# Optimization experiments

Hardware: AMD Instinct MI355X
Metric: run time of the kernel (lower is better)

The kernel has to match this reference:

```python
import jax, jax.numpy as jnp
import numpy as np

EMBED = 1024
HEADS = 16
HEAD_DIM = EMBED // HEADS
LN_EPS = 1e-5


def setup_inputs() -> dict:
    key = jax.random.key(0)
    ks = jax.random.split(key, 12)
    B, LQ, LK = 2, 2048, 2048
    s = 1.0 / np.sqrt(EMBED)
    inp = {
        "query_seq": jax.random.normal(ks[0], (B, LQ, EMBED), jnp.float32),
        "key_value_seq": jax.random.normal(ks[1], (B, LK, EMBED), jnp.float32),
        "prompt_size": 0,
        "Wq": jax.random.normal(ks[2], (EMBED, EMBED), jnp.float32) * s,
        "bq": jnp.zeros((EMBED,), jnp.float32),
        "Wk": jax.random.normal(ks[3], (EMBED, EMBED), jnp.float32) * s,
        "bk": jnp.zeros((EMBED,), jnp.float32),
        "Wv": jax.random.normal(ks[4], (EMBED, EMBED), jnp.float32) * s,
        "bv": jnp.zeros((EMBED,), jnp.float32),
        "Wo": jax.random.normal(ks[5], (EMBED, EMBED), jnp.float32) * s,
        "bo": jnp.zeros((EMBED,), jnp.float32),
        "ln_gamma": jnp.ones((EMBED,), jnp.float32),
        "ln_beta": jnp.zeros((EMBED,), jnp.float32),
    }
    return inp


def _split_heads(x):
    B, L, _ = x.shape
    return x.reshape(B, L, HEADS, HEAD_DIM).transpose(0, 2, 1, 3)  # [B,H,L,Dh]


def reference(query_seq, key_value_seq, prompt_size, Wq, bq, Wk, bk, Wv, bv, Wo, bo, ln_gamma, ln_beta):
    # projections (torch nn.Linear: x @ W.T + b)
    q = _split_heads(query_seq @ Wq.T + bq)
    k = _split_heads(key_value_seq @ Wk.T + bk)
    v = _split_heads(key_value_seq @ Wv.T + bv)
    # naive attention: full score matrix, softmax over keys
    scores = jnp.einsum("bhqd,bhkd->bhqk", q, k) / np.sqrt(HEAD_DIM).astype(np.float32)
    attn = jax.nn.softmax(scores, axis=-1)
    ctx = jnp.einsum("bhqk,bhkd->bhqd", attn, v)
    B, H, LQ, Dh = ctx.shape
    ctx = ctx.transpose(0, 2, 1, 3).reshape(B, LQ, H * Dh)
    out = ctx @ Wo.T + bo
    # residual + LayerNorm
    x = out + query_seq
    mu = jnp.mean(x, axis=-1, keepdims=True)
    var = jnp.var(x, axis=-1, keepdims=True)
    return (x - mu) * jax.lax.rsqrt(var + LN_EPS) * ln_gamma + ln_beta
```

## Files before the change

### kernel.cpp

```cpp
#include <hip/hip_runtime.h>

typedef unsigned short u16;
typedef unsigned int u32;
typedef __attribute__((ext_vector_type(8))) __bf16 bf16x8;
typedef __attribute__((ext_vector_type(4))) float f32x4;
typedef __attribute__((ext_vector_type(16))) float f32x16;

#define EMBED 1024
#define NB 2
#define LQ 2048
#define HEADS 16
#define DH 64
#define QSCALE 0.18033688011112042f

__device__ __forceinline__ u16 f2bf(float f) {
  u32 u = __float_as_uint(f);
  u32 r = (u + 0x7FFFu + ((u >> 16) & 1u)) >> 16;
  return (u16)r;
}

__device__ __forceinline__ void glds16(const void* g, void* l) {
  __builtin_amdgcn_global_load_lds((const __attribute__((address_space(1))) void*)g,
                                   (__attribute__((address_space(3))) void*)l, 16, 0, 0);
}

__device__ __forceinline__ f32x4 mfma16(bf16x8 a, bf16x8 b, f32x4 c) {
  return __builtin_amdgcn_mfma_f32_16x16x32_bf16(a, b, c, 0, 0, 0);
}
__device__ __forceinline__ f32x16 mfma32(bf16x8 a, bf16x8 b, f32x16 c) {
  return __builtin_amdgcn_mfma_f32_32x32x16_bf16(a, b, c, 0, 0, 0);
}

__device__ __forceinline__ void pl32(u32& a, u32& b) {
  asm("v_permlane32_swap_b32 %0, %1" : "+v"(a), "+v"(b));
}

__device__ __forceinline__ u32 packbf(float a, float b) {
  return __builtin_amdgcn_perm(__float_as_uint(b), __float_as_uint(a), 0x07060302u);
}

__global__ __launch_bounds__(256) void cast_kernel(
    const float* __restrict__ q, const float* __restrict__ kv,
    const float* __restrict__ wq, const float* __restrict__ wk,
    const float* __restrict__ wv, const float* __restrict__ wo,
    u16* __restrict__ qb, u16* __restrict__ kvb, u16* __restrict__ wqb,
    u16* __restrict__ wkb, u16* __restrict__ wvb, u16* __restrict__ wob) {
  int bid = blockIdx.x;
  const float* src;
  u16* dst;
  long base;
  if (bid < 2048) {
    src = q; dst = qb; base = (long)bid * 2048;
  } else if (bid < 4096) {
    src = kv; dst = kvb; base = (long)(bid - 2048) * 2048;
  } else {
    int wsel = (bid - 4096) >> 9;
    int wb = (bid - 4096) & 511;
    if (wsel == 0) { src = wq; dst = wqb; }
    else if (wsel == 1) { src = wk; dst = wkb; }
    else if (wsel == 2) { src = wv; dst = wvb; }
    else { src = wo; dst = wob; }
    base = (long)wb * 2048;
  }
  long e = base + (long)threadIdx.x * 8;
  float4 f0 = *(const float4*)(src + e);
  float4 f1 = *(const float4*)(src + e + 4);
  uint4 o;
  o.x = (u32)f2bf(f0.x) | ((u32)f2bf(f0.y) << 16);
  o.y = (u32)f2bf(f0.z) | ((u32)f2bf(f0.w) << 16);
  o.z = (u32)f2bf(f1.x) | ((u32)f2bf(f1.y) << 16);
  o.w = (u32)f2bf(f1.z) | ((u32)f2bf(f1.w) << 16);
  *(uint4*)(dst + e) = o;
}

template <int IT>
__device__ __forceinline__ void gemm_core(
    u16* As, u16* Bs, const u16* __restrict__ A, const u16* __restrict__ W,
    const float* __restrict__ bias, const float* __restrict__ resid,
    void* __restrict__ outp, int mode, int bx, int by) {
  const int K = EMBED;
  const int TM = IT * 32;
  const int tid = threadIdx.x;
  const int lane = tid & 63;
  const int wv = tid >> 6;
  const int wm = wv >> 1, wn = wv & 1;
  const int l16 = lane & 15, quad = lane >> 4;
  const long tile_m = (long)bx * TM;
  const long tile_n = (long)by * 128;

  f32x4 z4 = {0.f, 0.f, 0.f, 0.f};
  f32x4 acc[IT][4];
#pragma unroll
  for (int i = 0; i < IT; i++)
#pragma unroll
    for (int j = 0; j < 4; j++) acc[i][j] = z4;

  for (int k0 = 0; k0 < K; k0 += 64) {
#pragma unroll
    for (int it = 0; it < TM / 32; it++) {
      int lin = it * 256 + tid;
      int row = lin >> 3, cc = lin & 7;
      glds16(A + (tile_m + row) * K + k0 + ((cc ^ (row & 7)) << 3), As + lin * 8);
    }
#pragma unroll
    for (int it = 0; it < 4; it++) {
      int lin = it * 256 + tid;
      int row = lin >> 3, cc = lin & 7;
      glds16(W + (tile_n + row) * K + k0 + ((cc ^ (row & 7)) << 3), Bs + lin * 8);
    }
    __syncthreads();
    bf16x8 af[IT][2], bfr[4][2];
#pragma unroll
    for (int i = 0; i < IT; i++) {
      int row = wm * (IT * 16) + i * 16 + l16;
#pragma unroll
      for (int ki = 0; ki < 2; ki++)
        af[i][ki] = *(const bf16x8*)(As + row * 64 + (((ki * 4 + quad) ^ (row & 7)) << 3));
    }
#pragma unroll
    for (int j = 0; j < 4; j++) {
      int row = wn * 64 + j * 16 + l16;
#pragma unroll
      for (int ki = 0; ki < 2; ki++)
        bfr[j][ki] = *(const bf16x8*)(Bs + row * 64 + (((ki * 4 + quad) ^ (row & 7)) << 3));
    }
#pragma unroll
    for (int ki = 0; ki < 2; ki++)
#pragma unroll
      for (int i = 0; i < IT; i++)
#pragma unroll
        for (int j = 0; j < 4; j++) acc[i][j] = mfma16(af[i][ki], bfr[j][ki], acc[i][j]);
    __syncthreads();
  }

#pragma unroll
  for (int j = 0; j < 4; j++) {
    int gn = (int)tile_n + wn * 64 + j * 16 + l16;
    float bv = bias[gn];
#pragma unroll
    for (int i = 0; i < IT; i++) {
      long gm0 = tile_m + wm * (IT * 16) + i * 16 + quad * 4;
      if (mode == 3) {
#pragma unroll
        for (int r = 0; r < 4; r++) {
          long idx = (gm0 + r) * EMBED + gn;
          ((float*)outp)[idx] = acc[i][j][r] + bv + resid[idx];
        }
      } else if (mode == 2) {
        int b = (int)(gm0 >> 11), l = (int)(gm0 & 2047);
        int hh = gn >> 6, dh = gn & 63;
        uint2 pk;
        pk.x = (u32)f2bf(acc[i][j][0] + bv) | ((u32)f2bf(acc[i][j][1] + bv) << 16);
        pk.y = (u32)f2bf(acc[i][j][2] + bv) | ((u32)f2bf(acc[i][j][3] + bv) << 16);
        *(uint2*)((u16*)outp + (long)((b * HEADS + hh) * DH + dh) * LQ + l) = pk;
      } else {
#pragma unroll
        for (int r = 0; r < 4; r++) {
          long gm = gm0 + r;
          float v = acc[i][j][r] + bv;
          if (mode == 0) v *= QSCALE;
          int b = (int)(gm >> 11), l = (int)(gm & 2047);
          int hh = gn >> 6, dh = gn & 63;
          ((u16*)outp)[(long)((b * HEADS + hh) * LQ + l) * DH + dh] = f2bf(v);
        }
      }
    }
  }
}

__global__ __launch_bounds__(256) void qkv_kernel(
    const u16* __restrict__ qb, const u16* __restrict__ kvb,
    const u16* __restrict__ wqb, const u16* __restrict__ wkb, const u16* __restrict__ wvb,
    const float* __restrict__ bq, const float* __restrict__ bk, const float* __restrict__ bv,
    u16* __restrict__ Qh, u16* __restrict__ Kh, u16* __restrict__ Vt) {
  __shared__ u16 As[128 * 64];
  __shared__ u16 Bs[128 * 64];
  if (blockIdx.z == 0)      gemm_core<4>(As, Bs, qb,  wqb, bq, nullptr, Qh, 0, blockIdx.x, blockIdx.y);
  else if (blockIdx.z == 1) gemm_core<4>(As, Bs, kvb, wkb, bk, nullptr, Kh, 1, blockIdx.x, blockIdx.y);
  else                      gemm_core<4>(As, Bs, kvb, wvb, bv, nullptr, Vt, 2, blockIdx.x, blockIdx.y);
}

__global__ __launch_bounds__(256) void oproj_kernel(
    const u16* __restrict__ ctx, const u16* __restrict__ wob,
    const float* __restrict__ bo, const float* __restrict__ resid, float* __restrict__ out) {
  __shared__ u16 As[64 * 64];
  __shared__ u16 Bs[128 * 64];
  gemm_core<2>(As, Bs, ctx, wob, bo, resid, out, 3, blockIdx.x, blockIdx.y);
}

__global__ __launch_bounds__(256, 2) void attn_kernel(
    const u16* __restrict__ Qh, const u16* __restrict__ Kh,
    const u16* __restrict__ Vt, u16* __restrict__ ctx) {
  __shared__ u16 Qs[128 * 64];
  __shared__ u16 KVs[3][2][64 * 64];
  const int tid = threadIdx.x;
  const int lane = tid & 63;
  const int wv = tid >> 6;
  const int l32 = lane & 31, h = lane >> 5;
  const int qt = blockIdx.x, bh = blockIdx.y;
  const long qoff = (long)bh * (LQ * DH) + (long)qt * (128 * DH);
  const long koff = (long)bh * (LQ * DH);
  const long voff = (long)bh * (DH * LQ);
  const int qbase = wv * 32;

#define STAGE_KV(t, N)                                                          \
  do {                                                                          \
    _Pragma("unroll") for (int it = 0; it < 2; it++) {                          \
      int lin = it * 256 + tid;                                                 \
      int row = lin >> 3, cc = lin & 7;                                         \
      glds16(Kh + koff + (long)((t) * 64 + row) * 64 + ((cc ^ (row & 7)) << 3), \
             &KVs[N][0][0] + lin * 8);                                          \
      glds16(Vt + voff + (long)row * LQ + (t) * 64 + ((cc ^ (row & 7)) << 3),   \
             &KVs[N][1][0] + lin * 8);                                          \
    }                                                                           \
  } while (0)

#pragma unroll
  for (int it = 0; it < 4; it++) {
    int lin = it * 256 + tid;
    int row = lin >> 3, cc = lin & 7;
    glds16(Qh + qoff + row * 64 + ((cc ^ (row & 7)) << 3), Qs + lin * 8);
  }
  STAGE_KV(0, 0);
  STAGE_KV(1, 1);
  __syncthreads();

  bf16x8 bq[4];
  {
    int row = qbase + l32;
#pragma unroll
    for (int ks = 0; ks < 4; ks++)
      bq[ks] = *(const bf16x8*)(Qs + row * 64 + (((ks * 2 + h) ^ (row & 7)) << 3));
  }

  f32x16 z16 = {0.f, 0.f, 0.f, 0.f, 0.f, 0.f, 0.f, 0.f,
                0.f, 0.f, 0.f, 0.f, 0.f, 0.f, 0.f, 0.f};
  f32x16 ot[2];
  ot[0] = z16;
  ot[1] = z16;
  f32x16 st[2];
  uint2 pk[2][4];
  float2 ls2 = {0.f, 0.f};

#define DO_S(C)                                                                  \
  do {                                                                           \
    st[0] = z16;                                                                 \
    st[1] = z16;                                                                 \
    __builtin_amdgcn_s_setprio(1);                                               \
    _Pragma("unroll") for (int ks = 0; ks < 4; ks++) {                           \
      _Pragma("unroll") for (int mt = 0; mt < 2; mt++) {                         \
        int row = mt * 32 + l32;                                                 \
        bf16x8 ak = *(const bf16x8*)(&KVs[C][0][0] + row * 64 +                  \
                                     (((ks * 2 + h) ^ (row & 7)) << 3));         \
        st[mt] = mfma32(ak, bq[ks], st[mt]);                                     \
      }                                                                          \
    }                                                                            \
    __builtin_amdgcn_s_setprio(0);                                               \
  } while (0)

#define DO_SM()                                                                  \
  do {                                                                           \
    _Pragma("unroll") for (int mt = 0; mt < 2; mt++) {                           \
      _Pragma("unroll") for (int g = 0; g < 4; g++) {                            \
        float p0 = __builtin_amdgcn_exp2f(st[mt][g * 4 + 0]);                    \
        float p1 = __builtin_amdgcn_exp2f(st[mt][g * 4 + 1]);                    \
        float p2 = __builtin_amdgcn_exp2f(st[mt][g * 4 + 2]);                    \
        float p3 = __builtin_amdgcn_exp2f(st[mt][g * 4 + 3]);                    \
        ls2.x += p0 + p2;                                                        \
        ls2.y += p1 + p3;                                                        \
        pk[mt][g].x = packbf(p0, p1);                                            \
        pk[mt][g].y = packbf(p2, p3);                                            \
      }                                                                          \
    }                                                                            \
  } while (0)

#define DO_PV(P)                                                                 \
  do {                                                                           \
    _Pragma("unroll") for (int s = 0; s < 4; s++) {                              \
      uint2 wa = pk[s >> 1][(s & 1) * 2];                                        \
      uint2 wb = pk[s >> 1][(s & 1) * 2 + 1];                                    \
      u32 a0 = wa.x, b0 = wb.x, a1 = wa.y, b1 = wb.y;                            \
      pl32(a0, b0);                                                              \
      pl32(a1, b1);                                                              \
      union { u32 u[4]; bf16x8 v; } bp;                                          \
      bp.u[0] = a0;                                                              \
      bp.u[1] = a1;                                                              \
      bp.u[2] = b0;                                                              \
      bp.u[3] = b1;                                                              \
      __builtin_amdgcn_s_setprio(1);                                             \
      _Pragma("unroll") for (int mt2 = 0; mt2 < 2; mt2++) {                      \
        int row = mt2 * 32 + l32;                                                \
        bf16x8 av = *(const bf16x8*)(&KVs[P][1][0] + row * 64 +                  \
                                     ((((s << 1) + h) ^ (row & 7)) << 3));       \
        ot[mt2] = mfma32(av, bp.v, ot[mt2]);                                     \
      }                                                                          \
      __builtin_amdgcn_s_setprio(0);                                             \
    }                                                                            \
  } while (0)

#define AITER(kt, P, C, N)                                                       \
  do {                                                                           \
    if ((kt) + 1 < 32) STAGE_KV((kt) + 1, N);                                    \
    DO_SM();                                                                     \
    DO_S(C);                                                                     \
    DO_PV(P);                                                                    \
    __syncthreads();                                                             \
  } while (0)

  DO_S(0);

  AITER(1, 0, 1, 2);
  for (int k0 = 2; k0 < 32; k0 += 3) {
    AITER(k0, 1, 2, 0);
    AITER(k0 + 1, 2, 0, 1);
    AITER(k0 + 2, 0, 1, 2);
  }
  DO_SM();
  DO_PV(1);

#undef STAGE_KV
#undef DO_S
#undef DO_SM
#undef DO_PV
#undef AITER

  float lsum = ls2.x + ls2.y;
  lsum += __shfl_xor(lsum, 32);
  float inv = 1.0f / lsum;

  const int b = bh >> 4, head = bh & 15;
  int qrow = qt * 128 + qbase + l32;
  long base = (long)(b * LQ + qrow) * EMBED + head * DH;
#pragma unroll
  for (int mt = 0; mt < 2; mt++) {
#pragma unroll
    for (int g = 0; g < 4; g++) {
      uint2 pkk;
      pkk.x = (u32)f2bf(ot[mt][g * 4 + 0] * inv) | ((u32)f2bf(ot[mt][g * 4 + 1] * inv) << 16);
      pkk.y = (u32)f2bf(ot[mt][g * 4 + 2] * inv) | ((u32)f2bf(ot[mt][g * 4 + 3] * inv) << 16);
      *(uint2*)(ctx + base + mt * 32 + g * 8 + 4 * h) = pkk;
    }
  }
}

__global__ __launch_bounds__(256) void ln_kernel(
    float* __restrict__ x, const float* __restrict__ gamma, const float* __restrict__ beta) {
  __shared__ float red[8];
  const int tid = threadIdx.x;
  const long row = blockIdx.x;
  float4 v = *(const float4*)(x + row * EMBED + tid * 4);
  float s = v.x + v.y + v.z + v.w;
  float sq = v.x * v.x + v.y * v.y + v.z * v.z + v.w * v.w;
#pragma unroll
  for (int off = 1; off < 64; off <<= 1) {
    s += __shfl_xor(s, off);
    sq += __shfl_xor(sq, off);
  }
  if ((tid & 63) == 0) {
    red[(tid >> 6) * 2] = s;
    red[(tid >> 6) * 2 + 1] = sq;
  }
  __syncthreads();
  s = red[0] + red[2] + red[4] + red[6];
  sq = red[1] + red[3] + red[5] + red[7];
  float mu = s * (1.f / EMBED);
  float var = sq * (1.f / EMBED) - mu * mu;
  float rstd = rsqrtf(var + 1e-5f);
  float4 g = *(const float4*)(gamma + tid * 4);
  float4 bt = *(const float4*)(beta + tid * 4);
  float4 ov;
  ov.x = (v.x - mu) * rstd * g.x + bt.x;
  ov.y = (v.y - mu) * rstd * g.y + bt.y;
  ov.z = (v.z - mu) * rstd * g.z + bt.z;
  ov.w = (v.w - mu) * rstd * g.w + bt.w;
  *(float4*)(x + row * EMBED + tid * 4) = ov;
}

extern "C" void kernel_launch(void* const* d_in, const int* in_sizes, int n_in,
                              void* d_out, int out_size, void* d_ws, size_t ws_size,
                              hipStream_t stream) {
  const float* q     = (const float*)d_in[0];
  const float* kv    = (const float*)d_in[1];
  const float* Wq    = (const float*)d_in[3];
  const float* bq    = (const float*)d_in[4];
  const float* Wk    = (const float*)d_in[5];
  const float* bk    = (const float*)d_in[6];
  const float* Wv    = (const float*)d_in[7];
  const float* bv    = (const float*)d_in[8];
  const float* Wo    = (const float*)d_in[9];
  const float* bo    = (const float*)d_in[10];
  const float* gamma = (const float*)d_in[11];
  const float* beta  = (const float*)d_in[12];

  char* ws = (char*)d_ws;
  u16* qb  = (u16*)(ws + (0l  << 20));
  u16* kvb = (u16*)(ws + (8l  << 20));
  u16* wqb = (u16*)(ws + (16l << 20));
  u16* wkb = (u16*)(ws + (18l << 20));
  u16* wvb = (u16*)(ws + (20l << 20));
  u16* wob = (u16*)(ws + (22l << 20));
  u16* Qh  = (u16*)(ws + (24l << 20));
  u16* Kh  = (u16*)(ws + (32l << 20));
  u16* Vt  = (u16*)(ws + (40l << 20));
  u16* ctx = (u16*)(ws + (48l << 20));
  float* out = (float*)d_out;

  cast_kernel<<<6144, 256, 0, stream>>>(q, kv, Wq, Wk, Wv, Wo, qb, kvb, wqb, wkb, wvb, wob);
  qkv_kernel<<<dim3(32, 8, 3), 256, 0, stream>>>(qb, kvb, wqb, wkb, wvb, bq, bk, bv, Qh, Kh, Vt);
  attn_kernel<<<dim3(16, 32), 256, 0, stream>>>(Qh, Kh, Vt, ctx);
  oproj_kernel<<<dim3(64, 8), 256, 0, stream>>>(ctx, wob, bo, q, out);
  ln_kernel<<<4096, 256, 0, stream>>>(out, gamma, beta);
}
```

Baseline: 222.4 us.

## Double-buffer attention scores to overlap QK MFMA with softmax; retune QKV tiles

The attention loop now computes the next tile's QK^T into one score buffer while the softmax reads the previous buffer, alternating two register sets with the loop unrolled by six. This lets matrix-core work overlap with exp2 and packing, at the cost of more live registers. The QKV GEMM switches to smaller 64-row tiles with double the grid and an occupancy hint, and both GEMMs load A/B fragments per k-substep to lower register pressure.

After: 247.7 us. +11.4%, slower.

```diff
diff --git a/kernel.cpp b/kernel.cpp
--- a/kernel.cpp
+++ b/kernel.cpp
@@ -109,27 +109,24 @@
       glds16(W + (tile_n + row) * K + k0 + ((cc ^ (row & 7)) << 3), Bs + lin * 8);
     }
     __syncthreads();
-    bf16x8 af[IT][2], bfr[4][2];
-#pragma unroll
-    for (int i = 0; i < IT; i++) {
-      int row = wm * (IT * 16) + i * 16 + l16;
-#pragma unroll
-      for (int ki = 0; ki < 2; ki++)
-        af[i][ki] = *(const bf16x8*)(As + row * 64 + (((ki * 4 + quad) ^ (row & 7)) << 3));
+#pragma unroll
+    for (int ki = 0; ki < 2; ki++) {
+      bf16x8 af[IT], bfr[4];
+#pragma unroll
+      for (int i = 0; i < IT; i++) {
+        int row = wm * (IT * 16) + i * 16 + l16;
+        af[i] = *(const bf16x8*)(As + row * 64 + (((ki * 4 + quad) ^ (row & 7)) << 3));
+      }
+#pragma unroll
+      for (int j = 0; j < 4; j++) {
+        int row = wn * 64 + j * 16 + l16;
+        bfr[j] = *(const bf16x8*)(Bs + row * 64 + (((ki * 4 + quad) ^ (row & 7)) << 3));
+      }
+#pragma unroll
+      for (int i = 0; i < IT; i++)
+#pragma unroll
+        for (int j = 0; j < 4; j++) acc[i][j] = mfma16(af[i], bfr[j], acc[i][j]);
     }
-#pragma unroll
-    for (int j = 0; j < 4; j++) {
-      int row = wn * 64 + j * 16 + l16;
-#pragma unroll
-      for (int ki = 0; ki < 2; ki++)
-        bfr[j][ki] = *(const bf16x8*)(Bs + row * 64 + (((ki * 4 + quad) ^ (row & 7)) << 3));
-    }
-#pragma unroll
-    for (int ki = 0; ki < 2; ki++)
-#pragma unroll
-      for (int i = 0; i < IT; i++)
-#pragma unroll
-        for (int j = 0; j < 4; j++) acc[i][j] = mfma16(af[i][ki], bfr[j][ki], acc[i][j]);
     __syncthreads();
   }
 
@@ -168,19 +165,19 @@
   }
 }
 
-__global__ __launch_bounds__(256) void qkv_kernel(
+__global__ __launch_bounds__(256, 4) void qkv_kernel(
     const u16* __restrict__ qb, const u16* __restrict__ kvb,
     const u16* __restrict__ wqb, const u16* __restrict__ wkb, const u16* __restrict__ wvb,
     const float* __restrict__ bq, const float* __restrict__ bk, const float* __restrict__ bv,
     u16* __restrict__ Qh, u16* __restrict__ Kh, u16* __restrict__ Vt) {
-  __shared__ u16 As[128 * 64];
+  __shared__ u16 As[64 * 64];
   __shared__ u16 Bs[128 * 64];
-  if (blockIdx.z == 0)      gemm_core<4>(As, Bs, qb,  wqb, bq, nullptr, Qh, 0, blockIdx.x, blockIdx.y);
-  else if (blockIdx.z == 1) gemm_core<4>(As, Bs, kvb, wkb, bk, nullptr, Kh, 1, blockIdx.x, blockIdx.y);
-  else                      gemm_core<4>(As, Bs, kvb, wvb, bv, nullptr, Vt, 2, blockIdx.x, blockIdx.y);
-}
-
-__global__ __launch_bounds__(256) void oproj_kernel(
+  if (blockIdx.z == 0)      gemm_core<2>(As, Bs, qb,  wqb, bq, nullptr, Qh, 0, blockIdx.x, blockIdx.y);
+  else if (blockIdx.z == 1) gemm_core<2>(As, Bs, kvb, wkb, bk, nullptr, Kh, 1, blockIdx.x, blockIdx.y);
+  else                      gemm_core<2>(As, Bs, kvb, wvb, bv, nullptr, Vt, 2, blockIdx.x, blockIdx.y);
+}
+
+__global__ __launch_bounds__(256, 4) void oproj_kernel(
     const u16* __restrict__ ctx, const u16* __restrict__ wob,
     const float* __restrict__ bo, const float* __restrict__ resid, float* __restrict__ out) {
   __shared__ u16 As[64 * 64];
@@ -238,34 +235,32 @@
   f32x16 ot[2];
   ot[0] = z16;
   ot[1] = z16;
-  f32x16 st[2];
+  f32x16 sta[2], stb[2];
   uint2 pk[2][4];
   float2 ls2 = {0.f, 0.f};
 
-#define DO_S(C)                                                                  \
+#define DO_S(C, ST)                                                              \
   do {                                                                           \
-    st[0] = z16;                                                                 \
-    st[1] = z16;                                                                 \
     __builtin_amdgcn_s_setprio(1);                                               \
     _Pragma("unroll") for (int ks = 0; ks < 4; ks++) {                           \
       _Pragma("unroll") for (int mt = 0; mt < 2; mt++) {                         \
         int row = mt * 32 + l32;                                                 \
         bf16x8 ak = *(const bf16x8*)(&KVs[C][0][0] + row * 64 +                  \
                                      (((ks * 2 + h) ^ (row & 7)) << 3));         \
-        st[mt] = mfma32(ak, bq[ks], st[mt]);                                     \
+        ST[mt] = mfma32(ak, bq[ks], (ks == 0) ? z16 : ST[mt]);                   \
       }                                                                          \
     }                                                                            \
     __builtin_amdgcn_s_setprio(0);                                               \
   } while (0)
 
-#define DO_SM()                                                                  \
+#define DO_SM(ST)                                                                \
   do {                                                                           \
     _Pragma("unroll") for (int mt = 0; mt < 2; mt++) {                           \
       _Pragma("unroll") for (int g = 0; g < 4; g++) {                            \
-        float p0 = __builtin_amdgcn_exp2f(st[mt][g * 4 + 0]);                    \
-        float p1 = __builtin_amdgcn_exp2f(st[mt][g * 4 + 1]);                    \
-        float p2 = __builtin_amdgcn_exp2f(st[mt][g * 4 + 2]);                    \
-        float p3 = __builtin_amdgcn_exp2f(st[mt][g * 4 + 3]);                    \
+        float p0 = __builtin_amdgcn_exp2f(ST[mt][g * 4 + 0]);                    \
+        float p1 = __builtin_amdgcn_exp2f(ST[mt][g * 4 + 1]);                    \
+        float p2 = __builtin_amdgcn_exp2f(ST[mt][g * 4 + 2]);                    \
+        float p3 = __builtin_amdgcn_exp2f(ST[mt][g * 4 + 3]);                    \
         ls2.x += p0 + p2;                                                        \
         ls2.y += p1 + p3;                                                        \
         pk[mt][g].x = packbf(p0, p1);                                            \
@@ -298,24 +293,27 @@
     }                                                                            \
   } while (0)
 
-#define AITER(kt, P, C, N)                                                       \
+#define AITER(kt, P, C, N, STW, STR)                                             \
   do {                                                                           \
     if ((kt) + 1 < 32) STAGE_KV((kt) + 1, N);                                    \
-    DO_SM();                                                                     \
-    DO_S(C);                                                                     \
+    DO_S(C, STW);                                                                \
+    DO_SM(STR);                                                                  \
     DO_PV(P);                                                                    \
     __syncthreads();                                                             \
   } while (0)
 
-  DO_S(0);
-
-  AITER(1, 0, 1, 2);
-  for (int k0 = 2; k0 < 32; k0 += 3) {
-    AITER(k0, 1, 2, 0);
-    AITER(k0 + 1, 2, 0, 1);
-    AITER(k0 + 2, 0, 1, 2);
-  }
-  DO_SM();
+  DO_S(0, sta);
+
+  AITER(1, 0, 1, 2, stb, sta);
+  for (int k0 = 2; k0 < 32; k0 += 6) {
+    AITER(k0 + 0, 1, 2, 0, sta, stb);
+    AITER(k0 + 1, 2, 0, 1, stb, sta);
+    AITER(k0 + 2, 0, 1, 2, sta, stb);
+    AITER(k0 + 3, 1, 2, 0, stb, sta);
+    AITER(k0 + 4, 2, 0, 1, sta, stb);
+    AITER(k0 + 5, 0, 1, 2, stb, sta);
+  }
+  DO_SM(stb);
   DO_PV(1);
 
 #undef STAGE_KV
@@ -406,7 +404,7 @@
   float* out = (float*)d_out;
 
   cast_kernel<<<6144, 256, 0, stream>>>(q, kv, Wq, Wk, Wv, Wo, qb, kvb, wqb, wkb, wvb, wob);
-  qkv_kernel<<<dim3(32, 8, 3), 256, 0, stream>>>(qb, kvb, wqb, wkb, wvb, bq, bk, bv, Qh, Kh, Vt);
+  qkv_kernel<<<dim3(64, 8, 3), 256, 0, stream>>>(qb, kvb, wqb, wkb, wvb, bq, bk, bv, Qh, Kh, Vt);
   attn_kernel<<<dim3(16, 32), 256, 0, stream>>>(Qh, Kh, Vt, ctx);
   oproj_kernel<<<dim3(64, 8), 256, 0, stream>>>(ctx, wob, bo, q, out);
   ln_kernel<<<4096, 256, 0, stream>>>(out, gamma, beta);
```
